# Kernel optimization log

Hardware: AMD Instinct MI355X
Metric: run time of the kernel (lower is better)

Reference implementation:

```python
import jax, jax.numpy as jnp
import numpy as np

B, F, L, P = 64, 512, 512, 96
HT, HF = 8, 8  # temporal / feature attention heads
EPS_ATTN = 1e-6
EPS_LN = 1e-5
EPS_REVIN = 1e-5


def _layernorm(x, g, b):
    m = x.mean(axis=-1, keepdims=True)
    v = x.var(axis=-1, keepdims=True)
    return (x - m) / jnp.sqrt(v + EPS_LN) * g + b


def _lin_attn(x, Wq, bq, Wk, bk, Wv, bv, Wo, bo, H):
    # x: (B, N, D). Katharopoulos linear attention with elu+1 feature map.
    Bz, N, D = x.shape
    hd = D // H

    def proj(W, b):
        return (x @ W.T + b).reshape(Bz, N, H, hd).transpose(0, 2, 1, 3)  # (B,H,N,hd)

    Q = jax.nn.elu(proj(Wq, bq)) + 1.0
    K = jax.nn.elu(proj(Wk, bk)) + 1.0
    V = proj(Wv, bv)
    KV = jnp.einsum('bhnd,bhne->bhde', K, V)           # (B,H,hd,hd)
    out = jnp.einsum('bhnd,bhde->bhne', Q, KV)         # (B,H,N,hd)
    Z = K.sum(axis=2)                                  # (B,H,hd)
    norm = jnp.einsum('bhnd,bhd->bhn', Q, Z)[..., None] + EPS_ATTN
    out = (out / norm).transpose(0, 2, 1, 3).reshape(Bz, N, D)
    return out @ Wo.T + bo


def setup_inputs() -> dict:
    key = jax.random.key(0)
    ks = jax.random.split(key, 32)
    s = 0.1  # xavier-ish gain

    def w(k, shape, fan):
        return jax.random.normal(k, shape, dtype=jnp.float32) * (s / np.sqrt(fan))

    inp = {
        'x': jax.random.normal(ks[0], (B, F, L), dtype=jnp.float32),
        # RevIN affine
        'rg': jnp.ones((1, 1, F), jnp.float32),
        'rb': jnp.zeros((1, 1, F), jnp.float32),
        # LayerNorms
        'n1g': jnp.ones((F,), jnp.float32), 'n1b': jnp.zeros((F,), jnp.float32),
        'n2g': jnp.ones((L,), jnp.float32), 'n2b': jnp.zeros((L,), jnp.float32),
        # temporal attention (dim=F)
        'tWq': w(ks[1], (F, F), F), 'tbq': jnp.zeros((F,), jnp.float32),
        'tWk': w(ks[2], (F, F), F), 'tbk': jnp.zeros((F,), jnp.float32),
        'tWv': w(ks[3], (F, F), F), 'tbv': jnp.zeros((F,), jnp.float32),
        'tWo': w(ks[4], (F, F), F), 'tbo': jnp.zeros((F,), jnp.float32),
        # feature attention (dim=L)
        'fWq': w(ks[5], (L, L), L), 'fbq': jnp.zeros((L,), jnp.float32),
        'fWk': w(ks[6], (L, L), L), 'fbk': jnp.zeros((L,), jnp.float32),
        'fWv': w(ks[7], (L, L), L), 'fbv': jnp.zeros((L,), jnp.float32),
        'fWo': w(ks[8], (L, L), L), 'fbo': jnp.zeros((L,), jnp.float32),
        # individual per-feature Linear bank: seq_len -> pred_len
        'Wlin': w(ks[9], (F, P, L), L), 'blin': jnp.zeros((F, P), jnp.float32),
        # projector F -> 1
        'Wproj': w(ks[10], (1, F), F), 'bproj': jnp.zeros((1,), jnp.float32),
    }
    return inp


def reference(x, rg, rb, n1g, n1b,
              tWq, tbq, tWk, tbk, tWv, tbv, tWo, tbo,
              n2g, n2b,
              fWq, fbq, fWk, fbk, fWv, fbv, fWo, fbo,
              Wlin, blin, Wproj, bproj):
    # (B, F, L) -> (B, L, F)
    h = x.transpose(0, 2, 1)
    # RevIN norm (stats detached, std is unbiased like torch.std)
    mean = jax.lax.stop_gradient(h.mean(axis=1, keepdims=True))
    std = jax.lax.stop_gradient(jnp.std(h, axis=1, keepdims=True, ddof=1) + EPS_REVIN)
    h = (h - mean) / std * rg + rb

    # Dual linear attention
    r = h
    h = _layernorm(h, n1g, n1b)
    h = _lin_attn(h, tWq, tbq, tWk, tbk, tWv, tbv, tWo, tbo, HT) + r
    h = h.transpose(0, 2, 1)  # (B, F, L)
    r = h
    h = _layernorm(h, n2g, n2b)
    h = _lin_attn(h, fWq, fbq, fWk, fbk, fWv, fbv, fWo, fbo, HF) + r
    # (module transposes back to (B,L,F) then LinearCrypto permutes to (B,F,L);
    #  we stay in (B,F,L))

    # individual per-feature linear: seq_len -> pred_len
    y = jnp.einsum('bfl,fpl->bfp', h, Wlin) + blin[None]  # (B,F,P)
    y = y.transpose(0, 2, 1)                              # (B,P,F)
    # RevIN denorm
    y = (y - rb) / rg
    y = y * std + mean
    # projector F -> 1
    out = y @ Wproj.T + bproj  # (B,P,1)
    return out[..., 0]
```

## Files before the change

### kernel.cpp

```cpp
#include <hip/hip_runtime.h>
#include <hip/hip_bf16.h>
#include <cstdint>
#include <cstddef>


#define EPS_ATTN 1e-6f
#define EPS_LN   1e-5f
#define EPS_REVIN 1e-5f

typedef __attribute__((ext_vector_type(8))) short bf16x8;
typedef __attribute__((ext_vector_type(4))) float f32x4;
typedef __attribute__((ext_vector_type(8))) unsigned short u16x8;

__device__ __forceinline__ float bf2f(unsigned short u) {
  unsigned int x = ((unsigned int)u) << 16;
  return __builtin_bit_cast(float, x);
}
__device__ __forceinline__ unsigned short f2bf(float f) {
  __hip_bfloat16 h = __float2bfloat16(f);
  return __builtin_bit_cast(unsigned short, h);
}
__device__ __forceinline__ void gload16(const void* g, void* l) {
  __builtin_amdgcn_global_load_lds(
      (const __attribute__((address_space(1))) void*)g,
      (__attribute__((address_space(3))) void*)l, 16, 0, 0);
}

__global__ __launch_bounds__(256) void revin_xn_k(const float* __restrict__ x,
                                                  const float* __restrict__ rg,
                                                  const float* __restrict__ rb,
                                                  float* __restrict__ meanb,
                                                  float* __restrict__ stdb,
                                                  unsigned short* __restrict__ xn) {
  int wid = threadIdx.x >> 6, lane = threadIdx.x & 63;
  int row = blockIdx.x * 4 + wid;
  const float* xr = x + (size_t)row * 512 + lane * 8;
  float4 a = *(const float4*)xr;
  float4 c = *(const float4*)(xr + 4);
  float s1 = a.x + a.y + a.z + a.w + c.x + c.y + c.z + c.w;
  float s2 = a.x * a.x + a.y * a.y + a.z * a.z + a.w * a.w +
             c.x * c.x + c.y * c.y + c.z * c.z + c.w * c.w;
#pragma unroll
  for (int off = 1; off < 64; off <<= 1) { s1 += __shfl_xor(s1, off); s2 += __shfl_xor(s2, off); }
  float m = s1 * (1.f / 512.f);
  float var = fmaxf((s2 - 512.f * m * m) * (1.f / 511.f), 0.f);
  float sd = sqrtf(var) + EPS_REVIN;
  int f = row & 511;
  float sc = rg[f] / sd;
  float of = rb[f] - m * sc;
  u16x8 o;
  o[0] = f2bf(a.x * sc + of); o[1] = f2bf(a.y * sc + of);
  o[2] = f2bf(a.z * sc + of); o[3] = f2bf(a.w * sc + of);
  o[4] = f2bf(c.x * sc + of); o[5] = f2bf(c.y * sc + of);
  o[6] = f2bf(c.z * sc + of); o[7] = f2bf(c.w * sc + of);
  *(u16x8*)(xn + (size_t)row * 512 + lane * 8) = o;
  if (lane == 0) { meanb[row] = m; stdb[row] = sd; }
}

__global__ __launch_bounds__(256) void transpose_bf_k(const unsigned short* __restrict__ xn,
                                                      unsigned short* __restrict__ h1) {
  __shared__ float T[64][65];
  int b = blockIdx.z, f0 = blockIdx.y * 64, l0 = blockIdx.x * 64;
  int tid = threadIdx.x;
  int fr = tid >> 3, l8 = (tid & 7) * 8;
#pragma unroll
  for (int p = 0; p < 2; ++p) {
    int f = p * 32 + fr;
    u16x8 v = *(const u16x8*)(xn + ((size_t)(b * 512 + f0 + f)) * 512 + l0 + l8);
#pragma unroll
    for (int j = 0; j < 8; ++j) T[l8 + j][f] = bf2f(v[j]);
  }
  __syncthreads();
#pragma unroll
  for (int p = 0; p < 2; ++p) {
    int l = p * 32 + (tid >> 3), f8 = (tid & 7) * 8;
    u16x8 o;
#pragma unroll
    for (int j = 0; j < 8; ++j) o[j] = f2bf(T[l][f8 + j]);
    *(u16x8*)(h1 + ((size_t)(b * 512 + l0 + l)) * 512 + f0 + f8) = o;
  }
}

__global__ __launch_bounds__(256) void ln_k(const unsigned short* __restrict__ in,
                                            const float* __restrict__ g,
                                            const float* __restrict__ bq,
                                            unsigned short* __restrict__ o16) {
  int row = blockIdx.x * 4 + (threadIdx.x >> 6);
  int lane = threadIdx.x & 63;
  u16x8 u = *(const u16x8*)(in + (size_t)row * 512 + lane * 8);
  float v[8];
#pragma unroll
  for (int j = 0; j < 8; ++j) v[j] = bf2f(u[j]);
  float s1 = 0.f, s2 = 0.f;
#pragma unroll
  for (int j = 0; j < 8; ++j) { s1 += v[j]; s2 += v[j] * v[j]; }
#pragma unroll
  for (int off = 1; off < 64; off <<= 1) { s1 += __shfl_xor(s1, off); s2 += __shfl_xor(s2, off); }
  float m = s1 * (1.f / 512.f);
  float var = fmaxf(s2 * (1.f / 512.f) - m * m, 0.f);
  float iv = 1.f / sqrtf(var + EPS_LN);
  float4 g0 = *(const float4*)(g + lane * 8);
  float4 g1 = *(const float4*)(g + lane * 8 + 4);
  float4 b0 = *(const float4*)(bq + lane * 8);
  float4 b1 = *(const float4*)(bq + lane * 8 + 4);
  u16x8 o;
  o[0] = f2bf((v[0] - m) * iv * g0.x + b0.x);
  o[1] = f2bf((v[1] - m) * iv * g0.y + b0.y);
  o[2] = f2bf((v[2] - m) * iv * g0.z + b0.z);
  o[3] = f2bf((v[3] - m) * iv * g0.w + b0.w);
  o[4] = f2bf((v[4] - m) * iv * g1.x + b1.x);
  o[5] = f2bf((v[5] - m) * iv * g1.y + b1.y);
  o[6] = f2bf((v[6] - m) * iv * g1.z + b1.z);
  o[7] = f2bf((v[7] - m) * iv * g1.w + b1.w);
  *(u16x8*)(o16 + (size_t)row * 512 + lane * 8) = o;
}

__global__ __launch_bounds__(256) void wconv_k(const float* w0, const float* w1,
                                               const float* w2, const float* w3,
                                               const float* w4, const float* w5,
                                               const float* w6, const float* w7,
                                               unsigned short* __restrict__ out) {
  const float* srcs[8] = {w0, w1, w2, w3, w4, w5, w6, w7};
  const float* s = srcs[blockIdx.y];
  size_t idx = (size_t)blockIdx.x * 2048 + threadIdx.x * 8;
  float4 v0 = *(const float4*)(s + idx);
  float4 v1 = *(const float4*)(s + idx + 4);
  u16x8 o;
  o[0] = f2bf(v0.x); o[1] = f2bf(v0.y); o[2] = f2bf(v0.z); o[3] = f2bf(v0.w);
  o[4] = f2bf(v1.x); o[5] = f2bf(v1.y); o[6] = f2bf(v1.z); o[7] = f2bf(v1.w);
  *(u16x8*)(out + (size_t)blockIdx.y * 262144 + idx) = o;
}

__device__ __forceinline__ void gemm_core(const unsigned short* __restrict__ A,
                                          const unsigned short* __restrict__ W,
                                          unsigned short* smem,
                                          f32x4 (&acc)[4][4],
                                          int m0, int wrow, int tid) {
  const int w = tid >> 6, lane = tid & 63;
  const int wr = w >> 1, wc = w & 1;
  const int r8 = lane >> 3, s8 = lane & 7, gslot = s8 ^ r8;
  const unsigned short* Ag = A + (size_t)(m0 + w * 32 + r8) * 512 + gslot * 8;
  const unsigned short* Wg = W + (size_t)(wrow + w * 32 + r8) * 512 + gslot * 8;
  unsigned short* Asw = smem + w * 2048;
  unsigned short* Bsw = smem + 8192 + w * 2048;
  for (int k0 = 0; k0 < 512; k0 += 64) {
#pragma unroll
    for (int c = 0; c < 4; ++c) {
      gload16(Ag + (size_t)c * 8 * 512 + k0, Asw + c * 512);
      gload16(Wg + (size_t)c * 8 * 512 + k0, Bsw + c * 512);
    }
    __syncthreads();
#pragma unroll
    for (int s = 0; s < 2; ++s) {
      bf16x8 fa[4], fb[4];
#pragma unroll
      for (int i = 0; i < 4; ++i) {
        int ra = wr * 64 + i * 16 + (lane & 15);
        int sa = (s * 4 + (lane >> 4)) ^ (ra & 7);
        fa[i] = *(const bf16x8*)&smem[ra * 64 + sa * 8];
        int rb = wc * 64 + i * 16 + (lane & 15);
        int sb = (s * 4 + (lane >> 4)) ^ (rb & 7);
        fb[i] = *(const bf16x8*)&smem[8192 + rb * 64 + sb * 8];
      }
#pragma unroll
      for (int i = 0; i < 4; ++i)
#pragma unroll
        for (int j = 0; j < 4; ++j)
          acc[i][j] = __builtin_amdgcn_mfma_f32_16x16x32_bf16(fa[i], fb[j], acc[i][j], 0, 0, 0);
    }
    __syncthreads();
  }
}

template <int TRANS, int ACT, int RES>
__device__ __forceinline__ void gemm_epilogue(f32x4 (&acc)[4][4],
                                              unsigned short* Cs,
                                              const float* __restrict__ bias,
                                              const unsigned short* __restrict__ resid,
                                              unsigned short* __restrict__ out,
                                              int m0, int n0, int tid) {
  const int w = tid >> 6, lane = tid & 63;
  const int wr = w >> 1, wc = w & 1;
  const int ro = (lane >> 4) * 4, c16 = lane & 15;
#pragma unroll
  for (int j = 0; j < 4; ++j) {
    int nl = wc * 64 + j * 16 + c16;
    float bi = bias[n0 + nl];
#pragma unroll
    for (int i = 0; i < 4; ++i) {
      int ml = wr * 64 + i * 16 + ro;
#pragma unroll
      for (int r = 0; r < 4; ++r) {
        float v = acc[i][j][r] + bi;
        if constexpr (ACT) v = (v > 0.f) ? v + 1.f : __expf(v);
        if constexpr (TRANS) Cs[nl * 136 + ml + r] = f2bf(v);
        else                 Cs[(ml + r) * 136 + nl] = f2bf(v);
      }
    }
  }
  __syncthreads();
  size_t rowbase; int colbase;
  if constexpr (TRANS) { rowbase = (size_t)((m0 >> 9) * 512 + n0); colbase = m0 & 511; }
  else                 { rowbase = (size_t)m0; colbase = n0; }
#pragma unroll
  for (int c = 0; c < 8; ++c) {
    int idx = c * 256 + tid;
    int rr = idx >> 4, c8 = (idx & 15) * 8;
    u16x8 v = *(const u16x8*)&Cs[rr * 136 + c8];
    size_t gaddr = (rowbase + rr) * 512 + colbase + c8;
    if constexpr (RES) {
      u16x8 rv = *(const u16x8*)(resid + gaddr);
#pragma unroll
      for (int q = 0; q < 8; ++q) v[q] = f2bf(bf2f(v[q]) + bf2f(rv[q]));
    }
    *(u16x8*)(out + gaddr) = v;
  }
}

template <int TRANS, int ACT, int RES>
__global__ __launch_bounds__(256, 4) void gemm_std_k(const unsigned short* __restrict__ A,
                                                     const unsigned short* __restrict__ W,
                                                     const float* __restrict__ bias,
                                                     const unsigned short* __restrict__ resid,
                                                     unsigned short* __restrict__ out) {
  __shared__ unsigned short smem[17408] __attribute__((aligned(16)));
  const int tid = threadIdx.x;
  const int bid = blockIdx.x;
  const int nb = (bid & 7) * 128 + (bid >> 3);
  const int m0 = (nb >> 2) * 128;
  const int n0 = (nb & 3) * 128;
  f32x4 acc[4][4] = {};
  gemm_core(A, W, smem, acc, m0, n0, tid);
  gemm_epilogue<TRANS, ACT, RES>(acc, smem, bias, resid, out, m0, n0, tid);
}

__global__ __launch_bounds__(256) void kv_mfma_k(const unsigned short* __restrict__ KT,
                                                 const unsigned short* __restrict__ VT,
                                                 unsigned short* __restrict__ KVTo,
                                                 float* __restrict__ Zo) {
  int bh = blockIdx.x;
  int tid = threadIdx.x, w = tid >> 6, lane = tid & 63;
  int r16 = lane & 15, g = lane >> 4;
  const unsigned short* vb = VT + ((size_t)bh * 64 + w * 16 + r16) * 512 + g * 8;
  const unsigned short* kb = KT + ((size_t)bh * 64 + r16) * 512 + g * 8;
  f32x4 acc[4] = {};
  float zp[4] = {};
  for (int n0 = 0; n0 < 512; n0 += 32) {
    bf16x8 vf = *(const bf16x8*)(vb + n0);
#pragma unroll
    for (int j = 0; j < 4; ++j) {
      bf16x8 kf = *(const bf16x8*)(kb + (size_t)j * 16 * 512 + n0);
#pragma unroll
      for (int q = 0; q < 8; ++q) zp[j] += bf2f((unsigned short)kf[q]);
      acc[j] = __builtin_amdgcn_mfma_f32_16x16x32_bf16(vf, kf, acc[j], 0, 0, 0);
    }
  }
  int e = w * 16 + g * 4;
  unsigned short* kvo = KVTo + (size_t)bh * 4096;
#pragma unroll
  for (int j = 0; j < 4; ++j)
#pragma unroll
    for (int r = 0; r < 4; ++r)
      kvo[(size_t)(e + r) * 64 + j * 16 + r16] = f2bf(acc[j][r]);
#pragma unroll
  for (int j = 0; j < 4; ++j) {
    zp[j] += __shfl_xor(zp[j], 16);
    zp[j] += __shfl_xor(zp[j], 32);
  }
  if (w == 0 && lane < 16) {
#pragma unroll
    for (int j = 0; j < 4; ++j) Zo[(size_t)bh * 64 + j * 16 + lane] = zp[j];
  }
}

__global__ __launch_bounds__(512) void attn_mfma_k(unsigned short* __restrict__ Q16,
                                                   const unsigned short* __restrict__ KVT,
                                                   const float* __restrict__ Z) {
  __shared__ unsigned short kvs[32768] __attribute__((aligned(16)));
  __shared__ float Zs[512];
  int tid = threadIdx.x;
  int b = blockIdx.x >> 2;
  int m0 = blockIdx.x * 128;
  const unsigned short* kg = KVT + (size_t)b * 32768;
#pragma unroll
  for (int t = 0; t < 8; ++t) {
    int c = tid + t * 512;
    int e = (c >> 3) & 63;
    u16x8 v = *(const u16x8*)(kg + (size_t)c * 8);
    *(u16x8*)((char*)kvs + ((c * 16) ^ ((e & 7) << 4))) = v;
  }
  Zs[tid] = Z[(size_t)b * 512 + tid];
  __syncthreads();

  int w = tid >> 6, lane = tid & 63;
  int r16 = lane & 15, g = lane >> 4;
  unsigned short* qrow = Q16 + (size_t)(m0 + w * 16 + r16) * 512;
  int orow0 = m0 + w * 16 + g * 4;

  for (int h = 0; h < 8; ++h) {
    bf16x8 q0 = *(const bf16x8*)(qrow + h * 64 + g * 8);
    bf16x8 q1 = *(const bf16x8*)(qrow + h * 64 + 32 + g * 8);
    const float* zh = Zs + h * 64;
    float np = 0.f;
#pragma unroll
    for (int q = 0; q < 8; ++q) np = fmaf(bf2f((unsigned short)q0[q]), zh[g * 8 + q], np);
#pragma unroll
    for (int q = 0; q < 8; ++q) np = fmaf(bf2f((unsigned short)q1[q]), zh[32 + g * 8 + q], np);

    f32x4 acc[4] = {};
#pragma unroll
    for (int j = 0; j < 4; ++j) {
      int e = j * 16 + r16;
      int byte0 = h * 8192 + e * 128;
      int sw = (e & 7) << 4;
      bf16x8 k0 = *(const bf16x8*)((char*)kvs + ((byte0 + g * 16) ^ sw));
      bf16x8 k1 = *(const bf16x8*)((char*)kvs + ((byte0 + 64 + g * 16) ^ sw));
      acc[j] = __builtin_amdgcn_mfma_f32_16x16x32_bf16(q0, k0, acc[j], 0, 0, 0);
      acc[j] = __builtin_amdgcn_mfma_f32_16x16x32_bf16(q1, k1, acc[j], 0, 0, 0);
    }
    np += __shfl_xor(np, 16);
    np += __shfl_xor(np, 32);
    float inv = 1.f / (np + EPS_ATTN);
    float inv4[4];
#pragma unroll
    for (int r = 0; r < 4; ++r) inv4[r] = __shfl(inv, g * 4 + r);
#pragma unroll
    for (int j = 0; j < 4; ++j)
#pragma unroll
      for (int r = 0; r < 4; ++r)
        Q16[(size_t)(orow0 + r) * 512 + h * 64 + j * 16 + r16] = f2bf(acc[j][r] * inv4[r]);
  }
}

__global__ __launch_bounds__(256) void feat_linear_k(const unsigned short* __restrict__ h3,
                                                     const float* __restrict__ Wlin,
                                                     const float* __restrict__ blin,
                                                     float* __restrict__ Y) {
  int f = blockIdx.x;
  __shared__ float Hs[64][65];
  __shared__ float Ws2[96][65];
  int tid = threadIdx.x;
  int tx = tid & 15, ty = tid >> 4;
  float acc[4][6] = {};
  for (int l0 = 0; l0 < 512; l0 += 64) {
    {
      int bb = tid >> 2, c = (tid & 3) * 16;
      const unsigned short* hp = h3 + ((size_t)bb * 512 + f) * 512 + l0 + c;
      u16x8 v0 = *(const u16x8*)hp;
      u16x8 v1 = *(const u16x8*)(hp + 8);
#pragma unroll
      for (int q = 0; q < 8; ++q) { Hs[bb][c + q] = bf2f(v0[q]); Hs[bb][c + 8 + q] = bf2f(v1[q]); }
    }
#pragma unroll
    for (int s = 0; s < 6; ++s) {
      int q = s * 256 + tid;
      int p = q >> 4, c = (q & 15) * 4;
      float4 v = *(const float4*)(Wlin + ((size_t)f * 96 + p) * 512 + l0 + c);
      Ws2[p][c] = v.x; Ws2[p][c + 1] = v.y; Ws2[p][c + 2] = v.z; Ws2[p][c + 3] = v.w;
    }
    __syncthreads();
#pragma unroll 8
    for (int l = 0; l < 64; ++l) {
      float hv[4], wv[6];
#pragma unroll
      for (int i = 0; i < 4; ++i) hv[i] = Hs[ty * 4 + i][l];
#pragma unroll
      for (int j = 0; j < 6; ++j) wv[j] = Ws2[tx * 6 + j][l];
#pragma unroll
      for (int i = 0; i < 4; ++i)
#pragma unroll
        for (int j = 0; j < 6; ++j) acc[i][j] = fmaf(hv[i], wv[j], acc[i][j]);
    }
    __syncthreads();
  }
#pragma unroll
  for (int i = 0; i < 4; ++i) {
    int b = ty * 4 + i;
#pragma unroll
    for (int j = 0; j < 6; ++j) {
      int p = tx * 6 + j;
      Y[((size_t)b * 512 + f) * 96 + p] = acc[i][j] + blin[f * 96 + p];
    }
  }
}

__global__ __launch_bounds__(256) void final_out_k(const float* __restrict__ Y,
                                                   const float* __restrict__ meanb,
                                                   const float* __restrict__ stdb,
                                                   const float* __restrict__ rg,
                                                   const float* __restrict__ rb,
                                                   const float* __restrict__ Wproj,
                                                   const float* __restrict__ bproj,
                                                   float* __restrict__ out) {
  int b = blockIdx.x;
  __shared__ float cs[512];
  __shared__ float kred[4];
  int t = threadIdx.x;
  float kpart = 0.f;
  for (int f = t; f < 512; f += 256) {
    float sd = stdb[b * 512 + f], mn = meanb[b * 512 + f];
    float g = rg[f], rbv = rb[f], wp = Wproj[f];
    float c = wp * sd / g;
    cs[f] = c;
    kpart += wp * mn - c * rbv;
  }
#pragma unroll
  for (int off = 32; off; off >>= 1) kpart += __shfl_down(kpart, off);
  int wid = t >> 6, lane = t & 63;
  if (lane == 0) kred[wid] = kpart;
  __syncthreads();
  float K = kred[0] + kred[1] + kred[2] + kred[3] + bproj[0];
  if (t < 96) {
    float acc = 0.f;
    for (int f = 0; f < 512; ++f) acc = fmaf(cs[f], Y[((size_t)b * 512 + f) * 96 + t], acc);
    out[b * 96 + t] = acc + K;
  }
}

extern "C" void kernel_launch(void* const* d_in, const int* in_sizes, int n_in,
                              void* d_out, int out_size, void* d_ws, size_t ws_size,
                              hipStream_t stream) {
  const float* x    = (const float*)d_in[0];
  const float* rg   = (const float*)d_in[1];
  const float* rb   = (const float*)d_in[2];
  const float* n1g  = (const float*)d_in[3];
  const float* n1b  = (const float*)d_in[4];
  const float* n2g  = (const float*)d_in[5];
  const float* n2b  = (const float*)d_in[6];
  const float* tWq  = (const float*)d_in[7];
  const float* tbq  = (const float*)d_in[8];
  const float* tWk  = (const float*)d_in[9];
  const float* tbk  = (const float*)d_in[10];
  const float* tWv  = (const float*)d_in[11];
  const float* tbv  = (const float*)d_in[12];
  const float* tWo  = (const float*)d_in[13];
  const float* tbo  = (const float*)d_in[14];
  const float* fWq  = (const float*)d_in[15];
  const float* fbq  = (const float*)d_in[16];
  const float* fWk  = (const float*)d_in[17];
  const float* fbk  = (const float*)d_in[18];
  const float* fWv  = (const float*)d_in[19];
  const float* fbv  = (const float*)d_in[20];
  const float* fWo  = (const float*)d_in[21];
  const float* fbo  = (const float*)d_in[22];
  const float* Wlin = (const float*)d_in[23];
  const float* blin = (const float*)d_in[24];
  const float* Wprj = (const float*)d_in[25];
  const float* bprj = (const float*)d_in[26];
  float* out = (float*)d_out;

  const size_t SZ = (size_t)64 * 512 * 512;
  char* p = (char*)d_ws;
  unsigned short* xn  = (unsigned short*)p; p += SZ * 2;
  unsigned short* h1  = (unsigned short*)p; p += SZ * 2;
  unsigned short* h2  = (unsigned short*)p; p += SZ * 2;
  unsigned short* h3  = (unsigned short*)p; p += SZ * 2;
  unsigned short* abf = (unsigned short*)p; p += SZ * 2;
  unsigned short* q16 = (unsigned short*)p; p += SZ * 2;
  unsigned short* k16 = (unsigned short*)p; p += SZ * 2;
  unsigned short* v16 = (unsigned short*)p; p += SZ * 2;
  unsigned short* wbf = (unsigned short*)p; p += (size_t)8 * 262144 * 2;
  unsigned short* kvt = (unsigned short*)p; p += (size_t)512 * 4096 * 2;
  float* z     = (float*)p;         p += (size_t)512 * 64 * 4;
  float* meanb = (float*)p;         p += 32768 * 4;
  float* stdb  = (float*)p;         p += 32768 * 4;
  float* ybuf  = (float*)abf;

  wconv_k<<<dim3(128, 8), 256, 0, stream>>>(tWq, tWk, tWv, tWo, fWq, fWk, fWv, fWo, wbf);
  revin_xn_k<<<8192, 256, 0, stream>>>(x, rg, rb, meanb, stdb, xn);
  transpose_bf_k<<<dim3(8, 8, 64), 256, 0, stream>>>(xn, h1);

  ln_k<<<8192, 256, 0, stream>>>(h1, n1g, n1b, abf);
  gemm_std_k<0, 1, 0><<<1024, 256, 0, stream>>>(abf, wbf + 0 * 262144, tbq, nullptr, q16);
  gemm_std_k<1, 1, 0><<<1024, 256, 0, stream>>>(abf, wbf + 1 * 262144, tbk, nullptr, k16);
  gemm_std_k<1, 0, 0><<<1024, 256, 0, stream>>>(abf, wbf + 2 * 262144, tbv, nullptr, v16);
  kv_mfma_k<<<512, 256, 0, stream>>>(k16, v16, kvt, z);
  attn_mfma_k<<<256, 512, 0, stream>>>(q16, kvt, z);
  gemm_std_k<1, 0, 1><<<1024, 256, 0, stream>>>(q16, wbf + 3 * 262144, tbo, xn, h2);

  ln_k<<<8192, 256, 0, stream>>>(h2, n2g, n2b, abf);
  gemm_std_k<0, 1, 0><<<1024, 256, 0, stream>>>(abf, wbf + 4 * 262144, fbq, nullptr, q16);
  gemm_std_k<1, 1, 0><<<1024, 256, 0, stream>>>(abf, wbf + 5 * 262144, fbk, nullptr, k16);
  gemm_std_k<1, 0, 0><<<1024, 256, 0, stream>>>(abf, wbf + 6 * 262144, fbv, nullptr, v16);
  kv_mfma_k<<<512, 256, 0, stream>>>(k16, v16, kvt, z);
  attn_mfma_k<<<256, 512, 0, stream>>>(q16, kvt, z);
  gemm_std_k<0, 0, 1><<<1024, 256, 0, stream>>>(q16, wbf + 7 * 262144, fbo, h2, h3);

  feat_linear_k<<<512, 256, 0, stream>>>(h3, Wlin, blin, ybuf);
  final_out_k<<<64, 256, 0, stream>>>(ybuf, meanb, stdb, rg, rb, Wprj, bprj, out);
}
```

Before: 425.2 us.

## Use bf16 MFMA with swizzled LDS tiles in per-feature linear kernel

Rewrites the per-feature seq-to-pred linear kernel to use 16x16x32 bf16 MFMA instructions instead of scalar FP32 FMAs. Activations are loaded straight into LDS with direct global-to-LDS loads, and the FP32 Wlin weights are converted to bf16 on the fly. Both tiles use an XOR-swizzled LDS layout to avoid bank conflicts. It trades FP32 weight precision in this projection for matrix-core throughput.

```diff
diff --git a/kernel.cpp b/kernel.cpp
--- a/kernel.cpp
+++ b/kernel.cpp
@@ -336,51 +336,55 @@
                                                      const float* __restrict__ Wlin,
                                                      const float* __restrict__ blin,
                                                      float* __restrict__ Y) {
-  int f = blockIdx.x;
-  __shared__ float Hs[64][65];
-  __shared__ float Ws2[96][65];
-  int tid = threadIdx.x;
-  int tx = tid & 15, ty = tid >> 4;
-  float acc[4][6] = {};
-  for (int l0 = 0; l0 < 512; l0 += 64) {
-    {
-      int bb = tid >> 2, c = (tid & 3) * 16;
-      const unsigned short* hp = h3 + ((size_t)bb * 512 + f) * 512 + l0 + c;
-      u16x8 v0 = *(const u16x8*)hp;
-      u16x8 v1 = *(const u16x8*)(hp + 8);
-#pragma unroll
-      for (int q = 0; q < 8; ++q) { Hs[bb][c + q] = bf2f(v0[q]); Hs[bb][c + 8 + q] = bf2f(v1[q]); }
-    }
-#pragma unroll
-    for (int s = 0; s < 6; ++s) {
-      int q = s * 256 + tid;
-      int p = q >> 4, c = (q & 15) * 4;
-      float4 v = *(const float4*)(Wlin + ((size_t)f * 96 + p) * 512 + l0 + c);
-      Ws2[p][c] = v.x; Ws2[p][c + 1] = v.y; Ws2[p][c + 2] = v.z; Ws2[p][c + 3] = v.w;
+  __shared__ unsigned short As[64 * 64] __attribute__((aligned(16)));
+  __shared__ unsigned short Bs[96 * 64] __attribute__((aligned(16)));
+  const int f = blockIdx.x;
+  const int tid = threadIdx.x;
+  const int w = tid >> 6, lane = tid & 63;
+  const int r16 = lane & 15, g = lane >> 4;
+  const int r8 = lane >> 3, s8 = lane & 7, gs = s8 ^ r8;
+
+  f32x4 acc[6] = {};
+  for (int k0 = 0; k0 < 512; k0 += 64) {
+#pragma unroll
+    for (int c = 0; c < 2; ++c) {
+      int row = w * 16 + c * 8 + r8;
+      gload16(h3 + ((size_t)row * 512 + f) * 512 + k0 + gs * 8,
+              As + (w * 16 + c * 8) * 64);
+    }
+#pragma unroll
+    for (int it = 0; it < 3; ++it) {
+      int idx = it * 256 + tid;
+      int pp = idx >> 3, sl = idx & 7;
+      const float* src = Wlin + ((size_t)f * 96 + pp) * 512 + k0 + sl * 8;
+      float4 v0 = *(const float4*)src;
+      float4 v1 = *(const float4*)(src + 4);
+      u16x8 o;
+      o[0] = f2bf(v0.x); o[1] = f2bf(v0.y); o[2] = f2bf(v0.z); o[3] = f2bf(v0.w);
+      o[4] = f2bf(v1.x); o[5] = f2bf(v1.y); o[6] = f2bf(v1.z); o[7] = f2bf(v1.w);
+      *(u16x8*)&Bs[pp * 64 + (sl ^ (pp & 7)) * 8] = o;
     }
     __syncthreads();
-#pragma unroll 8
-    for (int l = 0; l < 64; ++l) {
-      float hv[4], wv[6];
-#pragma unroll
-      for (int i = 0; i < 4; ++i) hv[i] = Hs[ty * 4 + i][l];
-#pragma unroll
-      for (int j = 0; j < 6; ++j) wv[j] = Ws2[tx * 6 + j][l];
-#pragma unroll
-      for (int i = 0; i < 4; ++i)
-#pragma unroll
-        for (int j = 0; j < 6; ++j) acc[i][j] = fmaf(hv[i], wv[j], acc[i][j]);
+#pragma unroll
+    for (int s = 0; s < 2; ++s) {
+      int arow = w * 16 + r16;
+      bf16x8 fa = *(const bf16x8*)&As[arow * 64 + (((s * 4 + g) ^ (arow & 7)) * 8)];
+#pragma unroll
+      for (int n = 0; n < 6; ++n) {
+        int brow = n * 16 + r16;
+        bf16x8 fb = *(const bf16x8*)&Bs[brow * 64 + (((s * 4 + g) ^ (brow & 7)) * 8)];
+        acc[n] = __builtin_amdgcn_mfma_f32_16x16x32_bf16(fa, fb, acc[n], 0, 0, 0);
+      }
     }
     __syncthreads();
   }
-#pragma unroll
-  for (int i = 0; i < 4; ++i) {
-    int b = ty * 4 + i;
-#pragma unroll
-    for (int j = 0; j < 6; ++j) {
-      int p = tx * 6 + j;
-      Y[((size_t)b * 512 + f) * 96 + p] = acc[i][j] + blin[f * 96 + p];
-    }
+  const int b0 = w * 16 + g * 4;
+#pragma unroll
+  for (int n = 0; n < 6; ++n) {
+    float bi = blin[f * 96 + n * 16 + r16];
+#pragma unroll
+    for (int r = 0; r < 4; ++r)
+      Y[((size_t)(b0 + r) * 512 + f) * 96 + n * 16 + r16] = acc[n][r] + bi;
   }
 }
 
```

Result: faster. 395.3 us (-7.0%).
